# Optimization experiments

Measured on AMD Instinct MI355X. Metric: run time of the kernel, lower is better.

Reference implementation:

```python
import jax, jax.numpy as jnp
import numpy as np

N = 100_000
E = 1_600_000
D_IN = 128
D_HID = 128
D_OUT = 16
K = 3  # PyG TAGConv default number of hops


def setup_inputs() -> dict:
    key = jax.random.key(0)
    ks = jax.random.split(key, 5)
    x = jax.random.normal(ks[0], (N, D_IN), dtype=jnp.float32)
    edge_index = jax.random.randint(ks[1], (2, E), 0, N, dtype=jnp.int32)
    # TAGConv has (K+1) bias-free linear layers + one shared bias per conv
    W1 = jax.random.normal(ks[2], (K + 1, D_IN, D_HID), dtype=jnp.float32) * 0.05
    b1 = jnp.zeros((D_HID,), dtype=jnp.float32)
    W2 = jax.random.normal(ks[3], (K + 1, D_HID, D_OUT), dtype=jnp.float32) * 0.05
    b2 = jnp.zeros((D_OUT,), dtype=jnp.float32)
    return {"x": x, "edge_index": edge_index, "W1": W1, "b1": b1, "W2": W2, "b2": b2}


def _tag_conv(x, src, dst, norm, W, b):
    # out = sum_{k=0..K} (A_norm^k x) @ W[k] + b
    out = x @ W[0]
    h = x
    for k in range(1, W.shape[0]):
        msg = h[src] * norm[:, None]                      # [E, d] gather
        h = jax.ops.segment_sum(msg, dst, num_segments=x.shape[0])  # scatter-add
        out = out + h @ W[k]
    return out + b


def reference(x, edge_index, W1, b1, W2, b2):
    src, dst = edge_index[0], edge_index[1]
    # gcn_norm without self-loops: deg over target nodes
    deg = jax.ops.segment_sum(jnp.ones((src.shape[0],), x.dtype), dst, num_segments=x.shape[0])
    dis = jnp.where(deg > 0, jax.lax.rsqrt(jnp.maximum(deg, 1.0)), 0.0).astype(x.dtype)
    norm = dis[src] * dis[dst]
    h = jax.nn.relu(_tag_conv(x, src, dst, norm, W1, b1))
    return _tag_conv(h, src, dst, norm, W2, b2)
```

## Files before the change

### kernel.cpp

```cpp
#include <hip/hip_runtime.h>

#define DF 128

typedef __attribute__((ext_vector_type(8))) short bf16x8;
typedef __attribute__((ext_vector_type(4))) float f32x4;

__device__ __forceinline__ ushort f2bf(float f) {
  uint u = __float_as_uint(f);
  u += 0x7fff + ((u >> 16) & 1);
  return (ushort)(u >> 16);
}
__device__ __forceinline__ float bfl(uint v) { return __uint_as_float(v << 16); }
__device__ __forceinline__ float bfh(uint v) { return __uint_as_float(v & 0xffff0000u); }
__device__ __forceinline__ float b2f(ushort s) { return __uint_as_float(((uint)s) << 16); }

__device__ __forceinline__ void gload16(const ushort* g, ushort* l) {
  __builtin_amdgcn_global_load_lds((const __attribute__((address_space(1))) void*)g,
                                   (__attribute__((address_space(3))) void*)l, 16, 0, 0);
}

__global__ __launch_bounds__(256) void prepw_k(const float* __restrict__ W1, const float* __restrict__ W2,
                                               ushort* __restrict__ W1f, ushort* __restrict__ W2f,
                                               ushort* __restrict__ Z3s, ushort* __restrict__ T,
                                               ushort* __restrict__ GBs3, ushort* __restrict__ F0,
                                               ushort* __restrict__ F1, int n) {
  int b = blockIdx.x, tid = threadIdx.x;
  if (b == 256) {
    if (tid < 128) {
      Z3s[(size_t)n * 128 + tid] = 0;
      T[(size_t)n * 128 + tid] = 0;
    }
    if (tid < 16) {
      GBs3[(size_t)n * 16 + tid] = 0;
      F0[(size_t)n * 16 + tid] = 0;
      F1[(size_t)n * 16 + tid] = 0;
    }
    return;
  }
  int t = b * 256 + tid;
  {
    int k = t >> 14, rem = t & 16383;
    int frag = rem >> 3, j = rem & 7;
    int nt = frag >> 8, ks = (frag >> 6) & 3, lane = frag & 63;
    int nn = nt * 16 + (lane & 15);
    int kk = ks * 32 + (lane >> 4) * 8 + j;
    W1f[t] = f2bf(W1[k * 16384 + kk * 128 + nn]);
  }
  if (t < 8192) {
    int frag = t >> 3, j = t & 7;
    int nt = frag >> 8, ks = (frag >> 6) & 3, lane = frag & 63;
    int kk = ks * 32 + (lane >> 4) * 8 + j;
    W2f[t] = f2bf(W2[nt * 2048 + kk * 16 + (lane & 15)]);
  }
}

__global__ __launch_bounds__(256) void k1_k(const float* __restrict__ x, const ushort* __restrict__ W1f,
                                            ushort* __restrict__ Z3, ushort* __restrict__ Z2,
                                            ushort* __restrict__ Z1, ushort* __restrict__ Z0,
                                            const int* __restrict__ dst, int e,
                                            int* __restrict__ deg_s, int* __restrict__ rank,
                                            int n, int GZ) {
  __shared__ ushort wbuf[16384];
  int b = blockIdx.x, tid = threadIdx.x;
  if (b >= GZ) {
    int i = (b - GZ) * 256 + tid;
    if (i < e) {
      int shard = (i >> 8) & 7;
      rank[i] = atomicAdd(&deg_s[(size_t)shard * n + dst[i]], 1);
    }
    return;
  }
  int wid = tid >> 6, lane = tid & 63;
  int l15 = lane & 15, kgrp = lane >> 4;
  int m0 = b * 128 + wid * 32 + l15;
  int m1 = m0 + 16;
  int mc0 = m0 < n ? m0 : n - 1;
  int mc1 = m1 < n ? m1 : n - 1;
  bf16x8 xf0[4], xf1[4];
#pragma unroll
  for (int ks = 0; ks < 4; ks++) {
    float4 a0 = *reinterpret_cast<const float4*>(x + (size_t)mc0 * 128 + ks * 32 + kgrp * 8);
    float4 a1 = *reinterpret_cast<const float4*>(x + (size_t)mc0 * 128 + ks * 32 + kgrp * 8 + 4);
    float4 b0 = *reinterpret_cast<const float4*>(x + (size_t)mc1 * 128 + ks * 32 + kgrp * 8);
    float4 b1v = *reinterpret_cast<const float4*>(x + (size_t)mc1 * 128 + ks * 32 + kgrp * 8 + 4);
    bf16x8 u, w;
    u[0] = (short)f2bf(a0.x); u[1] = (short)f2bf(a0.y); u[2] = (short)f2bf(a0.z); u[3] = (short)f2bf(a0.w);
    u[4] = (short)f2bf(a1.x); u[5] = (short)f2bf(a1.y); u[6] = (short)f2bf(a1.z); u[7] = (short)f2bf(a1.w);
    w[0] = (short)f2bf(b0.x); w[1] = (short)f2bf(b0.y); w[2] = (short)f2bf(b0.z); w[3] = (short)f2bf(b0.w);
    w[4] = (short)f2bf(b1v.x); w[5] = (short)f2bf(b1v.y); w[6] = (short)f2bf(b1v.z); w[7] = (short)f2bf(b1v.w);
    xf0[ks] = u; xf1[ks] = w;
  }
#pragma unroll
  for (int kk = 0; kk < 4; kk++) {
    const int k = 3 - kk;
    {
      const ushort* gsrc = W1f + (size_t)k * 16384;
#pragma unroll
      for (int it = 0; it < 8; it++) {
        int f = it * 256 + tid;
        gload16(gsrc + (size_t)f * 8, &wbuf[f * 8]);
      }
    }
    __syncthreads();
    f32x4 acc0[8], acc1[8];
#pragma unroll
    for (int nt = 0; nt < 8; nt++) { acc0[nt] = {0.f,0.f,0.f,0.f}; acc1[nt] = {0.f,0.f,0.f,0.f}; }
#pragma unroll
    for (int ks = 0; ks < 4; ks++) {
#pragma unroll
      for (int nt = 0; nt < 8; nt++) {
        bf16x8 wf = *reinterpret_cast<const bf16x8*>(&wbuf[((nt * 4 + ks) * 64 + lane) * 8]);
        acc0[nt] = __builtin_amdgcn_mfma_f32_16x16x32_bf16(wf, xf0[ks], acc0[nt], 0, 0, 0);
        acc1[nt] = __builtin_amdgcn_mfma_f32_16x16x32_bf16(wf, xf1[ks], acc1[nt], 0, 0, 0);
      }
    }
    ushort* Out = (k == 3) ? Z3 : (k == 2) ? Z2 : (k == 1) ? Z1 : Z0;
#pragma unroll
    for (int nt = 0; nt < 8; nt++) {
      int ncol = nt * 16 + kgrp * 4;
      if (m0 < n) {
        ushort4 st; st.x = f2bf(acc0[nt][0]); st.y = f2bf(acc0[nt][1]);
        st.z = f2bf(acc0[nt][2]); st.w = f2bf(acc0[nt][3]);
        *reinterpret_cast<ushort4*>(Out + (size_t)m0 * 128 + ncol) = st;
      }
      if (m1 < n) {
        ushort4 st; st.x = f2bf(acc1[nt][0]); st.y = f2bf(acc1[nt][1]);
        st.z = f2bf(acc1[nt][2]); st.w = f2bf(acc1[nt][3]);
        *reinterpret_cast<ushort4*>(Out + (size_t)m1 * 128 + ncol) = st;
      }
    }
    __syncthreads();
  }
}

__global__ __launch_bounds__(256) void reduce_k(const int* __restrict__ deg_s, int n,
                                                int* __restrict__ deg, int* __restrict__ P,
                                                float* __restrict__ dis) {
  int i = blockIdx.x * 256 + threadIdx.x;
  if (i >= n) return;
  int run = 0;
#pragma unroll
  for (int s = 0; s < 8; s++) {
    int v = deg_s[(size_t)s * n + i];
    P[(size_t)s * n + i] = run;
    run += v;
  }
  deg[i] = run;
  dis[i] = run > 0 ? rsqrtf((float)run) : 0.f;
}

__global__ __launch_bounds__(256) void scan1_k(const int* __restrict__ deg, int n, int* __restrict__ partials) {
  __shared__ int sm[256];
  int base = blockIdx.x * 1024;
  int s = 0;
#pragma unroll
  for (int j = 0; j < 4; j++) { int idx = base + threadIdx.x * 4 + j; if (idx < n) s += deg[idx]; }
  sm[threadIdx.x] = s; __syncthreads();
  for (int off = 128; off > 0; off >>= 1) {
    if (threadIdx.x < off) sm[threadIdx.x] += sm[threadIdx.x + off];
    __syncthreads();
  }
  if (threadIdx.x == 0) partials[blockIdx.x] = sm[0];
}

__global__ void scan2_k(int* partials, int nb) {
  if (threadIdx.x == 0 && blockIdx.x == 0) {
    int run = 0;
    for (int i = 0; i < nb; i++) { int v = partials[i]; partials[i] = run; run += v; }
  }
}

__global__ __launch_bounds__(256) void scan3_k(const int* __restrict__ deg, int n, int e,
                                               const int* __restrict__ partials,
                                               int* __restrict__ rowptr) {
  __shared__ int sm[256];
  int base = blockIdx.x * 1024;
  int loc[4]; int s = 0;
#pragma unroll
  for (int j = 0; j < 4; j++) {
    int idx = base + threadIdx.x * 4 + j;
    int v = (idx < n) ? deg[idx] : 0;
    loc[j] = s; s += v;
  }
  sm[threadIdx.x] = s; __syncthreads();
  int tsum = s;
  for (int off = 1; off < 256; off <<= 1) {
    int v = (threadIdx.x >= (unsigned)off) ? sm[threadIdx.x - off] : 0;
    __syncthreads();
    sm[threadIdx.x] += v;
    __syncthreads();
  }
  int excl = sm[threadIdx.x] - tsum + partials[blockIdx.x];
#pragma unroll
  for (int j = 0; j < 4; j++) {
    int idx = base + threadIdx.x * 4 + j;
    if (idx < n) rowptr[idx] = excl + loc[j];
  }
  if (blockIdx.x == 0 && threadIdx.x == 0) rowptr[n] = e;
}

__global__ __launch_bounds__(256) void k2_k(const int* __restrict__ src, const int* __restrict__ dst, int e,
                                            const int* __restrict__ rank, const int* __restrict__ rowptr,
                                            const int* __restrict__ P, int* __restrict__ colb,
                                            ushort* __restrict__ Z3, const float* __restrict__ dis,
                                            int n, int gE) {
  int b = blockIdx.x, tid = threadIdx.x;
  if (b < gE) {
    int i = b * 256 + tid;
    if (i < e) {
      int d = dst[i];
      int shard = (i >> 8) & 7;
      int p = rowptr[d] + P[(size_t)shard * n + d] + rank[i];
      colb[p] = src[i];
    }
  } else {
    int u = (b - gE) * 256 + tid;
    int i = u >> 4, seg = u & 15;
    if (i < n) {
      float d = dis[i];
      ushort* p = Z3 + (size_t)i * 128 + seg * 8;
      uint4 v = *reinterpret_cast<const uint4*>(p);
      uint4 o;
      o.x = (uint)f2bf(d * bfl(v.x)) | ((uint)f2bf(d * bfh(v.x)) << 16);
      o.y = (uint)f2bf(d * bfl(v.y)) | ((uint)f2bf(d * bfh(v.y)) << 16);
      o.z = (uint)f2bf(d * bfl(v.z)) | ((uint)f2bf(d * bfh(v.z)) << 16);
      o.w = (uint)f2bf(d * bfl(v.w)) | ((uint)f2bf(d * bfh(v.w)) << 16);
      *reinterpret_cast<uint4*>(p) = o;
    }
  }
}

__global__ __launch_bounds__(256) void hop_k(const ushort* __restrict__ hin, const ushort* __restrict__ zk,
                                             const float* __restrict__ b1, ushort* __restrict__ hout,
                                             const int* __restrict__ rowptr, const int* __restrict__ colb,
                                             const float* __restrict__ dis, int n, int last) {
  int node = blockIdx.x * 16 + (threadIdx.x >> 4);
  int gl = threadIdx.x & 15;
  if (node >= n) return;
  int e0 = rowptr[node], e1 = rowptr[node + 1];
  float a0 = 0.f, a1 = 0.f, a2 = 0.f, a3 = 0.f, a4 = 0.f, a5 = 0.f, a6 = 0.f, a7 = 0.f;
  for (int ee = e0; ee < e1; ee += 8) {
    int c[8];
#pragma unroll
    for (int j = 0; j < 8; j++) {
      int idx = ee + j;
      c[j] = idx < e1 ? colb[idx] : n;
    }
    uint4 v[8];
#pragma unroll
    for (int j = 0; j < 8; j++)
      v[j] = *reinterpret_cast<const uint4*>(hin + (size_t)c[j] * 128 + gl * 8);
#pragma unroll
    for (int j = 0; j < 8; j++) {
      a0 += bfl(v[j].x); a1 += bfh(v[j].x);
      a2 += bfl(v[j].y); a3 += bfh(v[j].y);
      a4 += bfl(v[j].z); a5 += bfh(v[j].z);
      a6 += bfl(v[j].w); a7 += bfh(v[j].w);
    }
  }
  float d = dis[node];
  uint4 zr = *reinterpret_cast<const uint4*>(zk + (size_t)node * 128 + gl * 8);
  float t0 = fmaf(d, a0, bfl(zr.x)), t1 = fmaf(d, a1, bfh(zr.x));
  float t2 = fmaf(d, a2, bfl(zr.y)), t3 = fmaf(d, a3, bfh(zr.y));
  float t4 = fmaf(d, a4, bfl(zr.z)), t5 = fmaf(d, a5, bfh(zr.z));
  float t6 = fmaf(d, a6, bfl(zr.w)), t7 = fmaf(d, a7, bfh(zr.w));
  uint4 st;
  if (last) {
    float4 bv0 = *reinterpret_cast<const float4*>(b1 + gl * 8);
    float4 bv1 = *reinterpret_cast<const float4*>(b1 + gl * 8 + 4);
    t0 = fmaxf(t0 + bv0.x, 0.f); t1 = fmaxf(t1 + bv0.y, 0.f);
    t2 = fmaxf(t2 + bv0.z, 0.f); t3 = fmaxf(t3 + bv0.w, 0.f);
    t4 = fmaxf(t4 + bv1.x, 0.f); t5 = fmaxf(t5 + bv1.y, 0.f);
    t6 = fmaxf(t6 + bv1.z, 0.f); t7 = fmaxf(t7 + bv1.w, 0.f);
    st.x = (uint)f2bf(t0) | ((uint)f2bf(t1) << 16);
    st.y = (uint)f2bf(t2) | ((uint)f2bf(t3) << 16);
    st.z = (uint)f2bf(t4) | ((uint)f2bf(t5) << 16);
    st.w = (uint)f2bf(t6) | ((uint)f2bf(t7) << 16);
  } else {
    st.x = (uint)f2bf(d * t0) | ((uint)f2bf(d * t1) << 16);
    st.y = (uint)f2bf(d * t2) | ((uint)f2bf(d * t3) << 16);
    st.z = (uint)f2bf(d * t4) | ((uint)f2bf(d * t5) << 16);
    st.w = (uint)f2bf(d * t6) | ((uint)f2bf(d * t7) << 16);
  }
  *reinterpret_cast<uint4*>(hout + (size_t)node * 128 + gl * 8) = st;
}

__global__ __launch_bounds__(256) void gemm_last_k(const ushort* __restrict__ h1, const ushort* __restrict__ W2f,
                                                   const float* __restrict__ dis,
                                                   ushort* __restrict__ GB, ushort* __restrict__ GBs3, int n) {
  int wid = threadIdx.x >> 6, lane = threadIdx.x & 63;
  int kgrp = lane >> 4;
  int m = blockIdx.x * 64 + wid * 16 + (lane & 15);
  int mc = m < n ? m : n - 1;
  float dm = dis[mc];
  bf16x8 xf[4];
#pragma unroll
  for (int ks = 0; ks < 4; ks++)
    xf[ks] = *reinterpret_cast<const bf16x8*>(h1 + (size_t)mc * 128 + ks * 32 + kgrp * 8);
#pragma unroll
  for (int nt = 0; nt < 4; nt++) {
    f32x4 acc = {0.f, 0.f, 0.f, 0.f};
#pragma unroll
    for (int ks = 0; ks < 4; ks++) {
      bf16x8 wf = *reinterpret_cast<const bf16x8*>(W2f + (size_t)((nt * 4 + ks) * 64 + lane) * 8);
      acc = __builtin_amdgcn_mfma_f32_16x16x32_bf16(wf, xf[ks], acc, 0, 0, 0);
    }
    if (m < n) {
      int ncol = nt * 16 + kgrp * 4;
      ushort4 st; st.x = f2bf(acc[0]); st.y = f2bf(acc[1]); st.z = f2bf(acc[2]); st.w = f2bf(acc[3]);
      *reinterpret_cast<ushort4*>(GB + (size_t)m * 64 + ncol) = st;
      if (nt == 3) {
        ushort4 ss; ss.x = f2bf(dm * acc[0]); ss.y = f2bf(dm * acc[1]);
        ss.z = f2bf(dm * acc[2]); ss.w = f2bf(dm * acc[3]);
        *reinterpret_cast<ushort4*>(GBs3 + (size_t)m * 16 + kgrp * 4) = ss;
      }
    }
  }
}

__global__ __launch_bounds__(256) void spmm16_k(const ushort* __restrict__ in,
                                                const ushort* __restrict__ addraw, int addstride,
                                                const float* __restrict__ b2,
                                                float* __restrict__ outf, ushort* __restrict__ outb,
                                                const int* __restrict__ rowptr, const int* __restrict__ colb,
                                                const float* __restrict__ dis, int n) {
  int t = blockIdx.x * 256 + threadIdx.x;
  int node = t >> 3, cp = t & 7;
  if (node >= n) return;
  int e0 = rowptr[node], e1 = rowptr[node + 1];
  float a0 = 0.f, a1 = 0.f;
  for (int ee = e0; ee < e1; ee += 4) {
    int c[4];
#pragma unroll
    for (int j = 0; j < 4; j++) {
      int idx = ee + j;
      c[j] = idx < e1 ? colb[idx] : n;
    }
    uint v[4];
#pragma unroll
    for (int j = 0; j < 4; j++)
      v[j] = *reinterpret_cast<const uint*>(in + (size_t)c[j] * 16 + cp * 2);
#pragma unroll
    for (int j = 0; j < 4; j++) { a0 += bfl(v[j]); a1 += bfh(v[j]); }
  }
  float d = dis[node];
  uint av = *reinterpret_cast<const uint*>(addraw + (size_t)node * addstride + cp * 2);
  float t0 = fmaf(d, a0, b2f((ushort)(av & 0xffff)));
  float t1 = fmaf(d, a1, b2f((ushort)(av >> 16)));
  if (outf) {
    float2 st; st.x = t0 + b2[cp * 2]; st.y = t1 + b2[cp * 2 + 1];
    *reinterpret_cast<float2*>(outf + (size_t)node * 16 + cp * 2) = st;
  } else {
    uint pk = (uint)f2bf(d * t0) | ((uint)f2bf(d * t1) << 16);
    *reinterpret_cast<uint*>(outb + (size_t)node * 16 + cp * 2) = pk;
  }
}

extern "C" void kernel_launch(void* const* d_in, const int* in_sizes, int n_in,
                              void* d_out, int out_size, void* d_ws, size_t ws_size,
                              hipStream_t stream) {
  const float* x  = (const float*)d_in[0];
  const int*   ei = (const int*)d_in[1];
  const float* W1 = (const float*)d_in[2];
  const float* b1 = (const float*)d_in[3];
  const float* W2 = (const float*)d_in[4];
  const float* b2 = (const float*)d_in[5];
  float* out = (float*)d_out;

  const int n = in_sizes[0] / DF;
  const int e = in_sizes[1] / 2;
  const int* srcp = ei;
  const int* dstp = ei + e;

  char* ws = (char*)d_ws;
  size_t off = 0;
  auto alloc = [&](size_t bytes) -> void* {
    void* p = ws + off;
    off += (bytes + 255) & ~(size_t)255;
    return p;
  };
  ushort* Z3s  = (ushort*)alloc((size_t)(n + 1) * 128 * 2);
  ushort* T    = (ushort*)alloc((size_t)(n + 1) * 128 * 2);
  ushort* Z2   = (ushort*)alloc((size_t)n * 128 * 2);
  ushort* Z1   = (ushort*)alloc((size_t)n * 128 * 2);
  ushort* Z0   = (ushort*)alloc((size_t)n * 128 * 2);
  int*   deg_s = (int*)alloc((size_t)8 * n * 4);
  int*   P     = (int*)alloc((size_t)8 * n * 4);
  int*   deg   = (int*)alloc((size_t)n * 4);
  float* dis   = (float*)alloc((size_t)n * 4);
  int*   rowptr= (int*)alloc((size_t)(n + 1) * 4);
  int*   rank  = (int*)alloc((size_t)e * 4);
  int*   partials = (int*)alloc(1024 * 4);
  int*   colb  = (int*)alloc((size_t)e * 4);
  ushort* W1f  = (ushort*)alloc(4 * 128 * 128 * 2);
  ushort* W2f  = (ushort*)alloc(64 * 128 * 2);
  ushort* GBs3 = (ushort*)alloc((size_t)(n + 1) * 16 * 2);
  ushort* F0   = (ushort*)alloc((size_t)(n + 1) * 16 * 2);
  ushort* F1   = (ushort*)alloc((size_t)(n + 1) * 16 * 2);
  ushort* Up = Z3s;
  ushort* h1 = T;
  ushort* GB = Z2;

  hipMemsetAsync(deg_s, 0, (size_t)8 * n * 4, stream);

  int gE = (e + 255) / 256;
  int gN = (n + 255) / 256;
  int nb = (n + 1023) / 1024;
  int GZ = (n + 127) / 128;

  prepw_k<<<257, 256, 0, stream>>>(W1, W2, W1f, W2f, Z3s, T, GBs3, F0, F1, n);
  k1_k<<<GZ + gE, 256, 0, stream>>>(x, W1f, Z3s, Z2, Z1, Z0, dstp, e, deg_s, rank, n, GZ);
  reduce_k<<<gN, 256, 0, stream>>>(deg_s, n, deg, P, dis);
  scan1_k<<<nb, 256, 0, stream>>>(deg, n, partials);
  scan2_k<<<1, 64, 0, stream>>>(partials, nb);
  scan3_k<<<nb, 256, 0, stream>>>(deg, n, e, partials, rowptr);
  int gScale = (n * 16 + 255) / 256;
  k2_k<<<gE + gScale, 256, 0, stream>>>(srcp, dstp, e, rank, rowptr, P, colb, Z3s, dis, n, gE);

  int gHop = (n + 15) / 16;
  int gGemm = (n + 63) / 64;
  int gS16 = (n * 8 + 255) / 256;

  hop_k<<<gHop, 256, 0, stream>>>(Z3s, Z2, nullptr, T, rowptr, colb, dis, n, 0);
  hop_k<<<gHop, 256, 0, stream>>>(T, Z1, nullptr, Up, rowptr, colb, dis, n, 0);
  hop_k<<<gHop, 256, 0, stream>>>(Up, Z0, b1, h1, rowptr, colb, dis, n, 1);
  gemm_last_k<<<gGemm, 256, 0, stream>>>(h1, W2f, dis, GB, GBs3, n);

  spmm16_k<<<gS16, 256, 0, stream>>>(GBs3, GB + 32, 64, nullptr, nullptr, F0, rowptr, colb, dis, n);
  spmm16_k<<<gS16, 256, 0, stream>>>(F0,   GB + 16, 64, nullptr, nullptr, F1, rowptr, colb, dis, n);
  spmm16_k<<<gS16, 256, 0, stream>>>(F1,   GB + 0,  64, b2, out, nullptr, rowptr, colb, dis, n);
}
```

Before: 406.5 us.

## Split hop gathers into column halves and read W1 fragments from global

Each hop SpMM is now run as two launches, each gathering a 64-column half of the 128-wide bf16 features with 8-byte loads. The aim is a smaller per-pass working set that stays in cache better, in exchange for reading rowptr and colb twice and paying extra launch overhead. Separately, the first GEMM drops its LDS staging of W1 and the barriers around it, loading weight fragments straight from global memory per nt tile. That cuts register use for the accumulators but relies on cache hits for the repeated weight reads.

Measured after the change: 404.7 us. Within noise of the previous version (-0.5%).

```diff
diff --git a/kernel.cpp b/kernel.cpp
--- a/kernel.cpp
+++ b/kernel.cpp
@@ -13,11 +13,6 @@
 __device__ __forceinline__ float bfl(uint v) { return __uint_as_float(v << 16); }
 __device__ __forceinline__ float bfh(uint v) { return __uint_as_float(v & 0xffff0000u); }
 __device__ __forceinline__ float b2f(ushort s) { return __uint_as_float(((uint)s) << 16); }
-
-__device__ __forceinline__ void gload16(const ushort* g, ushort* l) {
-  __builtin_amdgcn_global_load_lds((const __attribute__((address_space(1))) void*)g,
-                                   (__attribute__((address_space(3))) void*)l, 16, 0, 0);
-}
 
 __global__ __launch_bounds__(256) void prepw_k(const float* __restrict__ W1, const float* __restrict__ W2,
                                                ushort* __restrict__ W1f, ushort* __restrict__ W2f,
@@ -60,7 +55,6 @@
                                             const int* __restrict__ dst, int e,
                                             int* __restrict__ deg_s, int* __restrict__ rank,
                                             int n, int GZ) {
-  __shared__ ushort wbuf[16384];
   int b = blockIdx.x, tid = threadIdx.x;
   if (b >= GZ) {
     int i = (b - GZ) * 256 + tid;
@@ -93,43 +87,29 @@
 #pragma unroll
   for (int kk = 0; kk < 4; kk++) {
     const int k = 3 - kk;
-    {
-      const ushort* gsrc = W1f + (size_t)k * 16384;
-#pragma unroll
-      for (int it = 0; it < 8; it++) {
-        int f = it * 256 + tid;
-        gload16(gsrc + (size_t)f * 8, &wbuf[f * 8]);
+    const ushort* Wk = W1f + (size_t)k * 16384;
+    ushort* Out = (k == 3) ? Z3 : (k == 2) ? Z2 : (k == 1) ? Z1 : Z0;
+#pragma unroll
+    for (int nt = 0; nt < 8; nt++) {
+      f32x4 acc0 = {0.f, 0.f, 0.f, 0.f}, acc1 = {0.f, 0.f, 0.f, 0.f};
+#pragma unroll
+      for (int ks = 0; ks < 4; ks++) {
+        bf16x8 wf = *reinterpret_cast<const bf16x8*>(Wk + (size_t)((nt * 4 + ks) * 64 + lane) * 8);
+        acc0 = __builtin_amdgcn_mfma_f32_16x16x32_bf16(wf, xf0[ks], acc0, 0, 0, 0);
+        acc1 = __builtin_amdgcn_mfma_f32_16x16x32_bf16(wf, xf1[ks], acc1, 0, 0, 0);
       }
-    }
-    __syncthreads();
-    f32x4 acc0[8], acc1[8];
-#pragma unroll
-    for (int nt = 0; nt < 8; nt++) { acc0[nt] = {0.f,0.f,0.f,0.f}; acc1[nt] = {0.f,0.f,0.f,0.f}; }
-#pragma unroll
-    for (int ks = 0; ks < 4; ks++) {
-#pragma unroll
-      for (int nt = 0; nt < 8; nt++) {
-        bf16x8 wf = *reinterpret_cast<const bf16x8*>(&wbuf[((nt * 4 + ks) * 64 + lane) * 8]);
-        acc0[nt] = __builtin_amdgcn_mfma_f32_16x16x32_bf16(wf, xf0[ks], acc0[nt], 0, 0, 0);
-        acc1[nt] = __builtin_amdgcn_mfma_f32_16x16x32_bf16(wf, xf1[ks], acc1[nt], 0, 0, 0);
-      }
-    }
-    ushort* Out = (k == 3) ? Z3 : (k == 2) ? Z2 : (k == 1) ? Z1 : Z0;
-#pragma unroll
-    for (int nt = 0; nt < 8; nt++) {
       int ncol = nt * 16 + kgrp * 4;
       if (m0 < n) {
-        ushort4 st; st.x = f2bf(acc0[nt][0]); st.y = f2bf(acc0[nt][1]);
-        st.z = f2bf(acc0[nt][2]); st.w = f2bf(acc0[nt][3]);
+        ushort4 st; st.x = f2bf(acc0[0]); st.y = f2bf(acc0[1]);
+        st.z = f2bf(acc0[2]); st.w = f2bf(acc0[3]);
         *reinterpret_cast<ushort4*>(Out + (size_t)m0 * 128 + ncol) = st;
       }
       if (m1 < n) {
-        ushort4 st; st.x = f2bf(acc1[nt][0]); st.y = f2bf(acc1[nt][1]);
-        st.z = f2bf(acc1[nt][2]); st.w = f2bf(acc1[nt][3]);
+        ushort4 st; st.x = f2bf(acc1[0]); st.y = f2bf(acc1[1]);
+        st.z = f2bf(acc1[2]); st.w = f2bf(acc1[3]);
         *reinterpret_cast<ushort4*>(Out + (size_t)m1 * 128 + ncol) = st;
       }
     }
-    __syncthreads();
   }
 }
 
@@ -233,12 +213,13 @@
 __global__ __launch_bounds__(256) void hop_k(const ushort* __restrict__ hin, const ushort* __restrict__ zk,
                                              const float* __restrict__ b1, ushort* __restrict__ hout,
                                              const int* __restrict__ rowptr, const int* __restrict__ colb,
-                                             const float* __restrict__ dis, int n, int last) {
+                                             const float* __restrict__ dis, int n, int colhalf, int last) {
   int node = blockIdx.x * 16 + (threadIdx.x >> 4);
   int gl = threadIdx.x & 15;
   if (node >= n) return;
+  int cbase = colhalf * 64 + gl * 4;
   int e0 = rowptr[node], e1 = rowptr[node + 1];
-  float a0 = 0.f, a1 = 0.f, a2 = 0.f, a3 = 0.f, a4 = 0.f, a5 = 0.f, a6 = 0.f, a7 = 0.f;
+  float a0 = 0.f, a1 = 0.f, a2 = 0.f, a3 = 0.f;
   for (int ee = e0; ee < e1; ee += 8) {
     int c[8];
 #pragma unroll
@@ -246,43 +227,32 @@
       int idx = ee + j;
       c[j] = idx < e1 ? colb[idx] : n;
     }
-    uint4 v[8];
+    uint2 v[8];
 #pragma unroll
     for (int j = 0; j < 8; j++)
-      v[j] = *reinterpret_cast<const uint4*>(hin + (size_t)c[j] * 128 + gl * 8);
+      v[j] = *reinterpret_cast<const uint2*>(hin + (size_t)c[j] * 128 + cbase);
 #pragma unroll
     for (int j = 0; j < 8; j++) {
       a0 += bfl(v[j].x); a1 += bfh(v[j].x);
       a2 += bfl(v[j].y); a3 += bfh(v[j].y);
-      a4 += bfl(v[j].z); a5 += bfh(v[j].z);
-      a6 += bfl(v[j].w); a7 += bfh(v[j].w);
     }
   }
   float d = dis[node];
-  uint4 zr = *reinterpret_cast<const uint4*>(zk + (size_t)node * 128 + gl * 8);
+  uint2 zr = *reinterpret_cast<const uint2*>(zk + (size_t)node * 128 + cbase);
   float t0 = fmaf(d, a0, bfl(zr.x)), t1 = fmaf(d, a1, bfh(zr.x));
   float t2 = fmaf(d, a2, bfl(zr.y)), t3 = fmaf(d, a3, bfh(zr.y));
-  float t4 = fmaf(d, a4, bfl(zr.z)), t5 = fmaf(d, a5, bfh(zr.z));
-  float t6 = fmaf(d, a6, bfl(zr.w)), t7 = fmaf(d, a7, bfh(zr.w));
-  uint4 st;
+  uint2 st;
   if (last) {
-    float4 bv0 = *reinterpret_cast<const float4*>(b1 + gl * 8);
-    float4 bv1 = *reinterpret_cast<const float4*>(b1 + gl * 8 + 4);
-    t0 = fmaxf(t0 + bv0.x, 0.f); t1 = fmaxf(t1 + bv0.y, 0.f);
-    t2 = fmaxf(t2 + bv0.z, 0.f); t3 = fmaxf(t3 + bv0.w, 0.f);
-    t4 = fmaxf(t4 + bv1.x, 0.f); t5 = fmaxf(t5 + bv1.y, 0.f);
-    t6 = fmaxf(t6 + bv1.z, 0.f); t7 = fmaxf(t7 + bv1.w, 0.f);
+    float4 bv = *reinterpret_cast<const float4*>(b1 + cbase);
+    t0 = fmaxf(t0 + bv.x, 0.f); t1 = fmaxf(t1 + bv.y, 0.f);
+    t2 = fmaxf(t2 + bv.z, 0.f); t3 = fmaxf(t3 + bv.w, 0.f);
     st.x = (uint)f2bf(t0) | ((uint)f2bf(t1) << 16);
     st.y = (uint)f2bf(t2) | ((uint)f2bf(t3) << 16);
-    st.z = (uint)f2bf(t4) | ((uint)f2bf(t5) << 16);
-    st.w = (uint)f2bf(t6) | ((uint)f2bf(t7) << 16);
   } else {
     st.x = (uint)f2bf(d * t0) | ((uint)f2bf(d * t1) << 16);
     st.y = (uint)f2bf(d * t2) | ((uint)f2bf(d * t3) << 16);
-    st.z = (uint)f2bf(d * t4) | ((uint)f2bf(d * t5) << 16);
-    st.w = (uint)f2bf(d * t6) | ((uint)f2bf(d * t7) << 16);
-  }
-  *reinterpret_cast<uint4*>(hout + (size_t)node * 128 + gl * 8) = st;
+  }
+  *reinterpret_cast<uint2*>(hout + (size_t)node * 128 + cbase) = st;
 }
 
 __global__ __launch_bounds__(256) void gemm_last_k(const ushort* __restrict__ h1, const ushort* __restrict__ W2f,
@@ -421,9 +391,12 @@
   int gGemm = (n + 63) / 64;
   int gS16 = (n * 8 + 255) / 256;
 
-  hop_k<<<gHop, 256, 0, stream>>>(Z3s, Z2, nullptr, T, rowptr, colb, dis, n, 0);
-  hop_k<<<gHop, 256, 0, stream>>>(T, Z1, nullptr, Up, rowptr, colb, dis, n, 0);
-  hop_k<<<gHop, 256, 0, stream>>>(Up, Z0, b1, h1, rowptr, colb, dis, n, 1);
+  hop_k<<<gHop, 256, 0, stream>>>(Z3s, Z2, nullptr, T, rowptr, colb, dis, n, 0, 0);
+  hop_k<<<gHop, 256, 0, stream>>>(Z3s, Z2, nullptr, T, rowptr, colb, dis, n, 1, 0);
+  hop_k<<<gHop, 256, 0, stream>>>(T, Z1, nullptr, Up, rowptr, colb, dis, n, 0, 0);
+  hop_k<<<gHop, 256, 0, stream>>>(T, Z1, nullptr, Up, rowptr, colb, dis, n, 1, 0);
+  hop_k<<<gHop, 256, 0, stream>>>(Up, Z0, b1, h1, rowptr, colb, dis, n, 0, 1);
+  hop_k<<<gHop, 256, 0, stream>>>(Up, Z0, b1, h1, rowptr, colb, dis, n, 1, 1);
   gemm_last_k<<<gGemm, 256, 0, stream>>>(h1, W2f, dis, GB, GBs3, n);
 
   spmm16_k<<<gS16, 256, 0, stream>>>(GBs3, GB + 32, 64, nullptr, nullptr, F0, rowptr, colb, dis, n);
```
